# Kernel tuning notes

Measured on AMD Instinct MI355X. Metric: run time of the kernel, lower is better.

## Reference

```python
import jax, jax.numpy as jnp
import numpy as np

H = 8       # num_heads
D = 64      # inner_dim (per-head)
DM = 512    # input_dim == output_dim
EPS = 1e-5


def setup_inputs() -> dict:
    key = jax.random.key(0)
    ks = jax.random.split(key, 6)
    b, n = 2, 2048
    x = jax.random.normal(ks[0], (b, n, DM), dtype=jnp.float32)
    w_qkv = jax.random.normal(ks[1], (DM, 3 * H * D), dtype=jnp.float32) * (DM ** -0.5)
    head_mix = jax.random.normal(ks[2], (H, H), dtype=jnp.float32)
    ln_h_g = jnp.ones((H,), jnp.float32)
    ln_h_b = jnp.zeros((H,), jnp.float32)
    w_out = jax.random.normal(ks[3], (H * D, DM), dtype=jnp.float32) * ((H * D) ** -0.5)
    b_out = jnp.zeros((DM,), jnp.float32)
    ln_o_g = jnp.ones((DM,), jnp.float32)
    ln_o_b = jnp.zeros((DM,), jnp.float32)
    return {"x": x, "w_qkv": w_qkv, "head_mix": head_mix,
            "ln_h_g": ln_h_g, "ln_h_b": ln_h_b,
            "w_out": w_out, "b_out": b_out,
            "ln_o_g": ln_o_g, "ln_o_b": ln_o_b}


def reference(x, w_qkv, head_mix, ln_h_g, ln_h_b, w_out, b_out, ln_o_g, ln_o_b):
    b, n, _ = x.shape
    scale = D ** -0.5
    qkv = x @ w_qkv                                   # [b, n, 3*H*D]
    q, k, v = jnp.split(qkv, 3, axis=-1)
    def heads(t):
        return t.reshape(b, n, H, D).transpose(0, 2, 1, 3)  # [b, H, n, D]
    q, k, v = heads(q), heads(k), heads(v)
    dots = jnp.einsum('bhid,bhjd->bhij', q, k) * scale
    attn = jax.nn.softmax(dots, axis=-1)
    # talking-heads mix: bhij,hg->bgij
    attn = jnp.einsum('bhij,hg->bgij', attn, head_mix)
    # LayerNorm over the head axis (axis=1)
    mu = attn.mean(axis=1, keepdims=True)
    var = attn.var(axis=1, keepdims=True)
    attn = (attn - mu) * jax.lax.rsqrt(var + EPS)
    attn = attn * ln_h_g[None, :, None, None] + ln_h_b[None, :, None, None]
    out = jnp.einsum('bhij,bhjd->bhid', attn, v)      # [b, H, n, D]
    out = out.transpose(0, 2, 1, 3).reshape(b, n, H * D)
    out = out @ w_out + b_out                         # [b, n, DM]
    # LayerNorm over feature dim
    mo = out.mean(axis=-1, keepdims=True)
    vo = out.var(axis=-1, keepdims=True)
    out = (out - mo) * jax.lax.rsqrt(vo + EPS) * ln_o_g + ln_o_b
    out = (x + out).sum(axis=1)                       # [b, DM]
    return out, attn
```

## Files before the change

### kernel.cpp

```cpp
#include <hip/hip_runtime.h>
#include <hip/hip_bf16.h>

typedef __attribute__((ext_vector_type(8)))  short short8;
typedef __attribute__((ext_vector_type(16))) float f32x16;

#define LOG2E 1.44269504088896f
#define CS (0.125f * LOG2E)

static __device__ __forceinline__ short f2b(float f) {
  union { __hip_bfloat16 h; short s; } u; u.h = __float2bfloat16(f); return u.s;
}
static __device__ __forceinline__ f32x16 zf16() {
  f32x16 z;
#pragma unroll
  for (int i = 0; i < 16; ++i) z[i] = 0.f;
  return z;
}
static __device__ __forceinline__ f32x16 mfma32(short8 a, short8 b, f32x16 c) {
  return __builtin_amdgcn_mfma_f32_32x32x16_bf16(a, b, c, 0, 0, 0);
}

__global__ void k_convert(const float* __restrict__ x, const float* __restrict__ wqkv,
                          const float* __restrict__ wout,
                          short* __restrict__ xb, short* __restrict__ wqkvT,
                          short* __restrict__ woutT) {
  const int NX = 2 * 2048 * 512;
  const int NW = 512 * 1536;
  const int NO = 512 * 512;
  int i = blockIdx.x * 256 + threadIdx.x;
  if (i < NX) {
    xb[i] = f2b(x[i]);
  } else if (i < NX + NW) {
    int o = i - NX; int n = o >> 9; int k = o & 511;
    wqkvT[o] = f2b(wqkv[k * 1536 + n]);
  } else if (i < NX + NW + NO) {
    int o = i - NX - NW; int n = o >> 9; int k = o & 511;
    woutT[o] = f2b(wout[k * 512 + n]);
  }
}

__global__ void k_xsum(const float* __restrict__ x, float* __restrict__ outacc) {
  int blk = blockIdx.x;
  int b = blk >> 4, ch = blk & 15;
  int t = threadIdx.x;
  int f = t * 2;
  float s0 = 0.f, s1 = 0.f;
  const float* base = x + ((size_t)b * 2048 + (size_t)ch * 128) * 512;
  for (int r = 0; r < 128; ++r) {
    float2 v = *(const float2*)(base + (size_t)r * 512 + f);
    s0 += v.x; s1 += v.y;
  }
  atomicAdd(&outacc[b * 512 + f], s0);
  atomicAdd(&outacc[b * 512 + f + 1], s1);
}

__launch_bounds__(256)
__global__ void k_qkv(const short* __restrict__ xb, const short* __restrict__ wqkvT,
                      short* __restrict__ qg, short* __restrict__ kg,
                      short* __restrict__ vtmp) {
  __shared__ __align__(16) short As[128 * 64];
  __shared__ __align__(16) short Bs[128 * 64];
  int bx = blockIdx.x & 31;
  int by = blockIdx.x >> 5;
  int row0 = bx << 7, col0 = by << 7;
  int t = threadIdx.x, w = t >> 6, l = t & 63, li = l & 31, hi = l >> 5;
  int wr = w >> 1, wc = w & 1;
  f32x16 acc[2][2];
#pragma unroll
  for (int mi = 0; mi < 2; ++mi)
#pragma unroll
    for (int ni = 0; ni < 2; ++ni) acc[mi][ni] = zf16();

  for (int k0 = 0; k0 < 512; k0 += 64) {
    __syncthreads();
#pragma unroll
    for (int it = 0; it < 4; ++it) {
      int idx = t + it * 256;
      int r = idx >> 3, pc = idx & 7;
      int4 va = *(const int4*)(xb + (size_t)(row0 + r) * 512 + k0 + pc * 8);
      int dsto = (r * 128 + pc * 16) ^ ((r & 7) << 4);
      *(int4*)((char*)As + dsto) = va;
      int4 vb = *(const int4*)(wqkvT + (size_t)(col0 + r) * 512 + k0 + pc * 8);
      *(int4*)((char*)Bs + dsto) = vb;
    }
    __syncthreads();
#pragma unroll
    for (int kk = 0; kk < 4; ++kk) {
      short8 af[2], bfv[2];
#pragma unroll
      for (int mi = 0; mi < 2; ++mi) {
        int row = wr * 64 + mi * 32 + li;
        int byteo = (row * 128 + (kk * 2 + hi) * 16) ^ ((row & 7) << 4);
        af[mi] = *(const short8*)((char*)As + byteo);
      }
#pragma unroll
      for (int ni = 0; ni < 2; ++ni) {
        int col = wc * 64 + ni * 32 + li;
        int byteo = (col * 128 + (kk * 2 + hi) * 16) ^ ((col & 7) << 4);
        bfv[ni] = *(const short8*)((char*)Bs + byteo);
      }
#pragma unroll
      for (int mi = 0; mi < 2; ++mi)
#pragma unroll
        for (int ni = 0; ni < 2; ++ni)
          acc[mi][ni] = mfma32(af[mi], bfv[ni], acc[mi][ni]);
    }
  }
#pragma unroll
  for (int mi = 0; mi < 2; ++mi)
#pragma unroll
    for (int ni = 0; ni < 2; ++ni) {
      int colb = col0 + wc * 64 + ni * 32 + li;
      int sect = colb >> 9, rem = colb & 511, h = rem >> 6, d = rem & 63;
      short* dst = sect == 0 ? qg : (sect == 1 ? kg : vtmp);
#pragma unroll
      for (int r = 0; r < 16; ++r) {
        int row = row0 + wr * 64 + mi * 32 + ((r & 3) + ((r >> 2) << 3) + (hi << 2));
        int b = row >> 11, nn = row & 2047;
        dst[(((size_t)(b * 8 + h) * 2048 + nn) << 6) + d] = f2b(acc[mi][ni][r]);
      }
    }
}

__global__ void k_vt(const short* __restrict__ vtmp, short* __restrict__ vt) {
  __shared__ __align__(16) short tile[64 * 72];
  int blk = blockIdx.x;
  int bh = blk >> 5;
  int n0 = (blk & 31) << 6;
  int t = threadIdx.x;
#pragma unroll
  for (int it = 0; it < 2; ++it) {
    int idx = (t + it * 256) * 8;
    int r = idx >> 6, c = idx & 63;
    int4 v = *(const int4*)(vtmp + ((size_t)bh * 2048 + n0 + r) * 64 + c);
    *(int4*)(&tile[r * 72 + c]) = v;
  }
  __syncthreads();
#pragma unroll
  for (int it = 0; it < 2; ++it) {
    int idx = (t + it * 256) * 8;
    int d = idx >> 6, nn = idx & 63;
    short8 o;
#pragma unroll
    for (int j = 0; j < 8; ++j) o[j] = tile[(nn + j) * 72 + d];
    *(short8*)(vt + ((size_t)bh * 64 + d) * 2048 + n0 + nn) = o;
  }
}

__launch_bounds__(256)
__global__ void k_stats(const short* __restrict__ qg, const short* __restrict__ kg,
                        float* __restrict__ ml) {
  int w = threadIdx.x >> 6, l = threadIdx.x & 63, li = l & 31, hi = l >> 5;
  int wt = blockIdx.x * 4 + w;
  int b = wt >> 9, rem = wt & 511, h = rem >> 6, it = rem & 63;
  size_t bh = (size_t)(b * 8 + h) * 2048;
  int i = it * 32 + li;
  short8 q4[4];
#pragma unroll
  for (int kk = 0; kk < 4; ++kk)
    q4[kk] = *(const short8*)(qg + (bh + i) * 64 + kk * 16 + hi * 8);
  float m2 = -1e30f, ls = 0.f;
  for (int jt = 0; jt < 64; ++jt) {
    f32x16 s = zf16();
#pragma unroll
    for (int kk = 0; kk < 4; ++kk) {
      short8 kf = *(const short8*)(kg + (bh + jt * 32 + li) * 64 + kk * 16 + hi * 8);
      s = mfma32(kf, q4[kk], s);
    }
    float sv[16];
    float tm = -1e30f;
#pragma unroll
    for (int r = 0; r < 16; ++r) { sv[r] = s[r] * CS; tm = fmaxf(tm, sv[r]); }
    float mn = fmaxf(m2, tm);
    float acc = 0.f;
#pragma unroll
    for (int r = 0; r < 16; ++r) acc += exp2f(sv[r] - mn);
    ls = ls * exp2f(m2 - mn) + acc;
    m2 = mn;
  }
  float om = __shfl_xor(m2, 32, 64);
  float ol = __shfl_xor(ls, 32, 64);
  float mf = fmaxf(m2, om);
  float lf = ls * exp2f(m2 - mf) + ol * exp2f(om - mf);
  if (hi == 0) {
    float2 v = make_float2(mf, lf);
    *(float2*)(ml + (bh + i) * 2) = v;
  }
}

__launch_bounds__(512)
__global__ void k_attn(const short* __restrict__ qg, const short* __restrict__ kg,
                       const short* __restrict__ vt, const float* __restrict__ ml,
                       const float* __restrict__ mixg, const float* __restrict__ lnhg,
                       const float* __restrict__ lnhb, float* __restrict__ attn,
                       float* __restrict__ oh) {
  __shared__ __align__(16) float p_lds[8 * 32 * 33];
  __shared__ __align__(16) short a_lds[8 * 32 * 40];
  int t = threadIdx.x;
  int w = t >> 6, l = t & 63, li = l & 31, hi = l >> 5;
  int blk = blockIdx.x;
  int jg = blk & 3, itile = (blk >> 2) & 63, b = blk >> 8;
  int i0 = itile * 32;
  int h = w;
  size_t bh = (size_t)(b * 8 + h) * 2048;

  float mixr[64];
#pragma unroll
  for (int z = 0; z < 64; ++z) mixr[z] = mixg[z];
  float lg[8], lbv[8];
#pragma unroll
  for (int g = 0; g < 8; ++g) { lg[g] = lnhg[g]; lbv[g] = lnhb[g]; }

  short8 q4[4];
#pragma unroll
  for (int kk = 0; kk < 4; ++kk)
    q4[kk] = *(const short8*)(qg + (bh + i0 + li) * 64 + kk * 16 + hi * 8);
  float2 mlv = *(const float2*)(ml + (bh + i0 + li) * 2);
  float mI = mlv.x;
  float rl = 1.0f / mlv.y;

  f32x16 oacc[2];
  oacc[0] = zf16(); oacc[1] = zf16();

  int jj = t & 31;
  int ipb = (t >> 5) & 15;

  for (int jt = 0; jt < 16; ++jt) {
    int j0 = jg * 512 + jt * 32;
    f32x16 s = zf16();
#pragma unroll
    for (int kk = 0; kk < 4; ++kk) {
      short8 kf = *(const short8*)(kg + (bh + j0 + li) * 64 + kk * 16 + hi * 8);
      s = mfma32(kf, q4[kk], s);
    }
#pragma unroll
    for (int r = 0; r < 16; ++r) {
      float p = exp2f(fmaf(s[r], CS, -mI)) * rl;
      int jr = (r & 3) + ((r >> 2) << 3) + (hi << 2);
      p_lds[(h * 32 + jr) * 33 + li] = p;
    }
    __syncthreads();
#pragma unroll
    for (int pp = 0; pp < 2; ++pp) {
      int ip = ipb + pp * 16;
      float ph[8];
#pragma unroll
      for (int g = 0; g < 8; ++g) ph[g] = p_lds[(g * 32 + jj) * 33 + ip];
      float a[8];
#pragma unroll
      for (int g = 0; g < 8; ++g) {
        float a2 = 0.f;
#pragma unroll
        for (int hh = 0; hh < 8; ++hh) a2 = fmaf(ph[hh], mixr[hh * 8 + g], a2);
        a[g] = a2;
      }
      float mu = 0.f;
#pragma unroll
      for (int g = 0; g < 8; ++g) mu += a[g];
      mu *= 0.125f;
      float var = 0.f;
#pragma unroll
      for (int g = 0; g < 8; ++g) { float d2 = a[g] - mu; var = fmaf(d2, d2, var); }
      var *= 0.125f;
      float rs = rsqrtf(var + 1e-5f);
#pragma unroll
      for (int g = 0; g < 8; ++g) {
        float y = (a[g] - mu) * rs * lg[g] + lbv[g];
        attn[((size_t)(b * 8 + g) * 2048 + (size_t)(i0 + ip)) * 2048 + j0 + jj] = y;
        a_lds[(g * 32 + ip) * 40 + jj] = f2b(y);
      }
    }
    __syncthreads();
#pragma unroll
    for (int ks = 0; ks < 2; ++ks) {
      short8 af = *(const short8*)(&a_lds[(h * 32 + li) * 40 + ks * 16 + hi * 8]);
#pragma unroll
      for (int dt = 0; dt < 2; ++dt) {
        short8 vf = *(const short8*)(vt + ((size_t)(b * 8 + h) * 64 + dt * 32 + li) * 2048 + j0 + ks * 16 + hi * 8);
        oacc[dt] = mfma32(af, vf, oacc[dt]);
      }
    }
  }
#pragma unroll
  for (int dt = 0; dt < 2; ++dt)
#pragma unroll
    for (int r = 0; r < 16; ++r) {
      int ri = (r & 3) + ((r >> 2) << 3) + (hi << 2);
      atomicAdd(&oh[((size_t)(b * 2048 + i0 + ri)) * 512 + h * 64 + dt * 32 + li], oacc[dt][r]);
    }
}

__launch_bounds__(512)
__global__ void k_epi(const float* __restrict__ oh, const short* __restrict__ woutT,
                      const float* __restrict__ bo, const float* __restrict__ logv,
                      const float* __restrict__ lob, float* __restrict__ dout) {
  __shared__ __align__(16) short As[64 * 64];
  __shared__ float lnsum[64][4];
  __shared__ float lnsq[64][4];
  __shared__ float zsum[512];
  int t = threadIdx.x, w = t >> 6, l = t & 63, li = l & 31, hi = l >> 5;
  int rb = w >> 2, cb = w & 3;
  int m0 = blockIdx.x * 64;
  zsum[t] = 0.f;
  f32x16 acc[4];
#pragma unroll
  for (int ni = 0; ni < 4; ++ni) acc[ni] = zf16();

  for (int k0 = 0; k0 < 512; k0 += 64) {
    __syncthreads();
    {
      int r = t >> 3, c = (t & 7) * 8;
      float4 v0 = *(const float4*)(oh + (size_t)(m0 + r) * 512 + k0 + c);
      float4 v1 = *(const float4*)(oh + (size_t)(m0 + r) * 512 + k0 + c + 4);
      short8 o;
      o[0] = f2b(v0.x); o[1] = f2b(v0.y); o[2] = f2b(v0.z); o[3] = f2b(v0.w);
      o[4] = f2b(v1.x); o[5] = f2b(v1.y); o[6] = f2b(v1.z); o[7] = f2b(v1.w);
      int byteo = (r * 128 + c * 2) ^ ((r & 7) << 4);
      *(short8*)((char*)As + byteo) = o;
    }
    __syncthreads();
#pragma unroll
    for (int kk = 0; kk < 4; ++kk) {
      int rowA = rb * 32 + li;
      int byteo = (rowA * 128 + (kk * 2 + hi) * 16) ^ ((rowA & 7) << 4);
      short8 af = *(const short8*)((char*)As + byteo);
#pragma unroll
      for (int ni = 0; ni < 4; ++ni) {
        int n = cb * 128 + ni * 32 + li;
        short8 bfr = *(const short8*)(woutT + (size_t)n * 512 + k0 + kk * 16 + hi * 8);
        acc[ni] = mfma32(af, bfr, acc[ni]);
      }
    }
  }
  float bias[4], gg[4], b2[4];
#pragma unroll
  for (int ni = 0; ni < 4; ++ni) {
    int n = cb * 128 + ni * 32 + li;
    bias[ni] = bo[n]; gg[ni] = logv[n]; b2[ni] = lob[n];
  }
#pragma unroll
  for (int ni = 0; ni < 4; ++ni)
#pragma unroll
    for (int r = 0; r < 16; ++r) acc[ni][r] += bias[ni];

#pragma unroll
  for (int r = 0; r < 16; ++r) {
    float s = 0.f, q2 = 0.f;
#pragma unroll
    for (int ni = 0; ni < 4; ++ni) { float v = acc[ni][r]; s += v; q2 = fmaf(v, v, q2); }
    for (int d2 = 1; d2 < 32; d2 <<= 1) { s += __shfl_xor(s, d2); q2 += __shfl_xor(q2, d2); }
    int rw = rb * 32 + (r & 3) + ((r >> 2) << 3) + (hi << 2);
    if (li == 0) { lnsum[rw][cb] = s; lnsq[rw][cb] = q2; }
  }
  __syncthreads();
  float zp[4] = {0.f, 0.f, 0.f, 0.f};
#pragma unroll
  for (int r = 0; r < 16; ++r) {
    int rw = rb * 32 + (r & 3) + ((r >> 2) << 3) + (hi << 2);
    float s = lnsum[rw][0] + lnsum[rw][1] + lnsum[rw][2] + lnsum[rw][3];
    float q2 = lnsq[rw][0] + lnsq[rw][1] + lnsq[rw][2] + lnsq[rw][3];
    float mu = s * (1.f / 512.f);
    float var = q2 * (1.f / 512.f) - mu * mu;
    float rs = rsqrtf(var + 1e-5f);
#pragma unroll
    for (int ni = 0; ni < 4; ++ni) {
      float y = (acc[ni][r] - mu) * rs * gg[ni] + b2[ni];
      zp[ni] += y;
    }
  }
#pragma unroll
  for (int ni = 0; ni < 4; ++ni) zp[ni] += __shfl_xor(zp[ni], 32);
  if (hi == 0) {
#pragma unroll
    for (int ni = 0; ni < 4; ++ni) atomicAdd(&zsum[cb * 128 + ni * 32 + li], zp[ni]);
  }
  __syncthreads();
  int bsel = m0 >> 11;
  atomicAdd(&dout[bsel * 512 + t], zsum[t]);
}

extern "C" void kernel_launch(void* const* d_in, const int* in_sizes, int n_in,
                              void* d_out, int out_size, void* d_ws, size_t ws_size,
                              hipStream_t stream) {
  const float* x    = (const float*)d_in[0];
  const float* wqkv = (const float*)d_in[1];
  const float* mixg = (const float*)d_in[2];
  const float* lnhg = (const float*)d_in[3];
  const float* lnhb = (const float*)d_in[4];
  const float* wout = (const float*)d_in[5];
  const float* bo   = (const float*)d_in[6];
  const float* logv = (const float*)d_in[7];
  const float* lob  = (const float*)d_in[8];
  float* dout = (float*)d_out;
  char* ws = (char*)d_ws;
  short* xb    = (short*)(ws + 0);
  short* wqkvT = (short*)(ws + 4194304);
  short* woutT = (short*)(ws + 5767168);
  short* qg    = (short*)(ws + 6291456);
  short* kg    = (short*)(ws + 10485760);
  short* vtmp  = (short*)(ws + 14680064);
  short* vt    = (short*)(ws + 18874368);
  float* ml    = (float*)(ws + 23068672);
  float* oh    = (float*)(ws + 23330816);

  hipMemsetAsync(dout, 0, 1024 * sizeof(float), stream);
  hipMemsetAsync(oh, 0, (size_t)2 * 2048 * 512 * 4, stream);

  k_convert<<<12288, 256, 0, stream>>>(x, wqkv, wout, xb, wqkvT, woutT);
  k_xsum<<<32, 256, 0, stream>>>(x, dout);
  k_qkv<<<384, 256, 0, stream>>>(xb, wqkvT, qg, kg, vtmp);
  k_vt<<<512, 256, 0, stream>>>(vtmp, vt);
  k_stats<<<256, 256, 0, stream>>>(qg, kg, ml);
  k_attn<<<512, 512, 0, stream>>>(qg, kg, vt, ml, mixg, lnhg, lnhb, dout + 1024, oh);
  k_epi<<<64, 512, 0, stream>>>(oh, woutT, bo, logv, lob, dout);
}
```

Before: 555.1 us.

## Parallelize stats over waves, replace oh atomics with partial buffers, vectorize attn stores

```diff
diff --git a/kernel.cpp b/kernel.cpp
--- a/kernel.cpp
+++ b/kernel.cpp
@@ -18,6 +18,9 @@
 }
 static __device__ __forceinline__ f32x16 mfma32(short8 a, short8 b, f32x16 c) {
   return __builtin_amdgcn_mfma_f32_32x32x16_bf16(a, b, c, 0, 0, 0);
+}
+static __device__ __forceinline__ float rfl(float v) {
+  return __int_as_float(__builtin_amdgcn_readfirstlane(__float_as_int(v)));
 }
 
 __global__ void k_convert(const float* __restrict__ x, const float* __restrict__ wqkv,
@@ -150,9 +153,10 @@
 __launch_bounds__(256)
 __global__ void k_stats(const short* __restrict__ qg, const short* __restrict__ kg,
                         float* __restrict__ ml) {
-  int w = threadIdx.x >> 6, l = threadIdx.x & 63, li = l & 31, hi = l >> 5;
-  int wt = blockIdx.x * 4 + w;
-  int b = wt >> 9, rem = wt & 511, h = rem >> 6, it = rem & 63;
+  __shared__ float red[4][32][2];
+  int t = threadIdx.x, w = t >> 6, l = t & 63, li = l & 31, hi = l >> 5;
+  int blk = blockIdx.x;
+  int b = blk >> 9, rem = blk & 511, h = rem >> 6, it = rem & 63;
   size_t bh = (size_t)(b * 8 + h) * 2048;
   int i = it * 32 + li;
   short8 q4[4];
@@ -160,7 +164,7 @@
   for (int kk = 0; kk < 4; ++kk)
     q4[kk] = *(const short8*)(qg + (bh + i) * 64 + kk * 16 + hi * 8);
   float m2 = -1e30f, ls = 0.f;
-  for (int jt = 0; jt < 64; ++jt) {
+  for (int jt = w * 16; jt < w * 16 + 16; ++jt) {
     f32x16 s = zf16();
 #pragma unroll
     for (int kk = 0; kk < 4; ++kk) {
@@ -182,13 +186,22 @@
   float ol = __shfl_xor(ls, 32, 64);
   float mf = fmaxf(m2, om);
   float lf = ls * exp2f(m2 - mf) + ol * exp2f(om - mf);
-  if (hi == 0) {
-    float2 v = make_float2(mf, lf);
-    *(float2*)(ml + (bh + i) * 2) = v;
-  }
-}
-
-__launch_bounds__(512)
+  if (hi == 0) { red[w][li][0] = mf; red[w][li][1] = lf; }
+  __syncthreads();
+  if (t < 32) {
+    float m = red[0][t][0], s = red[0][t][1];
+#pragma unroll
+    for (int ww = 1; ww < 4; ++ww) {
+      float m1 = red[ww][t][0], s1 = red[ww][t][1];
+      float mn = fmaxf(m, m1);
+      s = s * exp2f(m - mn) + s1 * exp2f(m1 - mn);
+      m = mn;
+    }
+    *(float2*)(ml + (bh + it * 32 + t) * 2) = make_float2(m, s);
+  }
+}
+
+__launch_bounds__(512, 4)
 __global__ void k_attn(const short* __restrict__ qg, const short* __restrict__ kg,
                        const short* __restrict__ vt, const float* __restrict__ ml,
                        const float* __restrict__ mixg, const float* __restrict__ lnhg,
@@ -206,24 +219,23 @@
 
   float mixr[64];
 #pragma unroll
-  for (int z = 0; z < 64; ++z) mixr[z] = mixg[z];
+  for (int z = 0; z < 64; ++z) mixr[z] = rfl(mixg[z]);
   float lg[8], lbv[8];
 #pragma unroll
-  for (int g = 0; g < 8; ++g) { lg[g] = lnhg[g]; lbv[g] = lnhb[g]; }
+  for (int g = 0; g < 8; ++g) { lg[g] = rfl(lnhg[g]); lbv[g] = rfl(lnhb[g]); }
 
   short8 q4[4];
 #pragma unroll
   for (int kk = 0; kk < 4; ++kk)
     q4[kk] = *(const short8*)(qg + (bh + i0 + li) * 64 + kk * 16 + hi * 8);
   float2 mlv = *(const float2*)(ml + (bh + i0 + li) * 2);
-  float mI = mlv.x;
-  float rl = 1.0f / mlv.y;
+  float c0 = -(mlv.x + __log2f(mlv.y));
 
   f32x16 oacc[2];
   oacc[0] = zf16(); oacc[1] = zf16();
 
-  int jj = t & 31;
-  int ipb = (t >> 5) & 15;
+  int ii = t >> 4;
+  int jp = (t & 15) * 2;
 
   for (int jt = 0; jt < 16; ++jt) {
     int j0 = jg * 512 + jt * 32;
@@ -235,39 +247,49 @@
     }
 #pragma unroll
     for (int r = 0; r < 16; ++r) {
-      float p = exp2f(fmaf(s[r], CS, -mI)) * rl;
+      float p = exp2f(fmaf(s[r], CS, c0));
       int jr = (r & 3) + ((r >> 2) << 3) + (hi << 2);
       p_lds[(h * 32 + jr) * 33 + li] = p;
     }
     __syncthreads();
-#pragma unroll
-    for (int pp = 0; pp < 2; ++pp) {
-      int ip = ipb + pp * 16;
-      float ph[8];
-#pragma unroll
-      for (int g = 0; g < 8; ++g) ph[g] = p_lds[(g * 32 + jj) * 33 + ip];
-      float a[8];
+    {
+      float pf[8][2], a[8][2];
 #pragma unroll
       for (int g = 0; g < 8; ++g) {
-        float a2 = 0.f;
-#pragma unroll
-        for (int hh = 0; hh < 8; ++hh) a2 = fmaf(ph[hh], mixr[hh * 8 + g], a2);
-        a[g] = a2;
-      }
-      float mu = 0.f;
-#pragma unroll
-      for (int g = 0; g < 8; ++g) mu += a[g];
-      mu *= 0.125f;
-      float var = 0.f;
-#pragma unroll
-      for (int g = 0; g < 8; ++g) { float d2 = a[g] - mu; var = fmaf(d2, d2, var); }
-      var *= 0.125f;
-      float rs = rsqrtf(var + 1e-5f);
+        pf[g][0] = p_lds[(g * 32 + jp) * 33 + ii];
+        pf[g][1] = p_lds[(g * 32 + jp + 1) * 33 + ii];
+      }
 #pragma unroll
       for (int g = 0; g < 8; ++g) {
-        float y = (a[g] - mu) * rs * lg[g] + lbv[g];
-        attn[((size_t)(b * 8 + g) * 2048 + (size_t)(i0 + ip)) * 2048 + j0 + jj] = y;
-        a_lds[(g * 32 + ip) * 40 + jj] = f2b(y);
+#pragma unroll
+        for (int jb = 0; jb < 2; ++jb) {
+          float a2 = 0.f;
+#pragma unroll
+          for (int hh = 0; hh < 8; ++hh) a2 = fmaf(pf[hh][jb], mixr[hh * 8 + g], a2);
+          a[g][jb] = a2;
+        }
+      }
+      float mu[2], rs[2];
+#pragma unroll
+      for (int jb = 0; jb < 2; ++jb) {
+        float m2 = 0.f;
+#pragma unroll
+        for (int g = 0; g < 8; ++g) m2 += a[g][jb];
+        m2 *= 0.125f;
+        float var = 0.f;
+#pragma unroll
+        for (int g = 0; g < 8; ++g) { float d2 = a[g][jb] - m2; var = fmaf(d2, d2, var); }
+        var *= 0.125f;
+        mu[jb] = m2; rs[jb] = rsqrtf(var + 1e-5f);
+      }
+#pragma unroll
+      for (int g = 0; g < 8; ++g) {
+        float y0 = (a[g][0] - mu[0]) * rs[0] * lg[g] + lbv[g];
+        float y1 = (a[g][1] - mu[1]) * rs[1] * lg[g] + lbv[g];
+        *(float2*)(&attn[((size_t)(b * 8 + g) * 2048 + (size_t)(i0 + ii)) * 2048 + j0 + jp]) =
+            make_float2(y0, y1);
+        unsigned int pk = (unsigned short)f2b(y0) | ((unsigned int)(unsigned short)f2b(y1) << 16);
+        *(unsigned int*)(&a_lds[(g * 32 + ii) * 40 + jp]) = pk;
       }
     }
     __syncthreads();
@@ -281,12 +303,13 @@
       }
     }
   }
+  float* ohp = oh + (size_t)jg * (2 * 2048 * 512);
 #pragma unroll
   for (int dt = 0; dt < 2; ++dt)
 #pragma unroll
     for (int r = 0; r < 16; ++r) {
       int ri = (r & 3) + ((r >> 2) << 3) + (hi << 2);
-      atomicAdd(&oh[((size_t)(b * 2048 + i0 + ri)) * 512 + h * 64 + dt * 32 + li], oacc[dt][r]);
+      ohp[((size_t)(b * 2048 + i0 + ri)) * 512 + h * 64 + dt * 32 + li] = oacc[dt][r];
     }
 }
 
@@ -294,85 +317,88 @@
 __global__ void k_epi(const float* __restrict__ oh, const short* __restrict__ woutT,
                       const float* __restrict__ bo, const float* __restrict__ logv,
                       const float* __restrict__ lob, float* __restrict__ dout) {
-  __shared__ __align__(16) short As[64 * 64];
-  __shared__ float lnsum[64][4];
-  __shared__ float lnsq[64][4];
+  __shared__ __align__(16) short As[32 * 64];
+  __shared__ float lnsum[32][8];
+  __shared__ float lnsq[32][8];
   __shared__ float zsum[512];
+  const size_t NPART = (size_t)2 * 2048 * 512;
   int t = threadIdx.x, w = t >> 6, l = t & 63, li = l & 31, hi = l >> 5;
-  int rb = w >> 2, cb = w & 3;
-  int m0 = blockIdx.x * 64;
-  zsum[t] = 0.f;
-  f32x16 acc[4];
-#pragma unroll
-  for (int ni = 0; ni < 4; ++ni) acc[ni] = zf16();
+  int m0 = blockIdx.x * 32;
+  f32x16 acc[2];
+  acc[0] = zf16(); acc[1] = zf16();
 
   for (int k0 = 0; k0 < 512; k0 += 64) {
     __syncthreads();
     {
-      int r = t >> 3, c = (t & 7) * 8;
-      float4 v0 = *(const float4*)(oh + (size_t)(m0 + r) * 512 + k0 + c);
-      float4 v1 = *(const float4*)(oh + (size_t)(m0 + r) * 512 + k0 + c + 4);
-      short8 o;
-      o[0] = f2b(v0.x); o[1] = f2b(v0.y); o[2] = f2b(v0.z); o[3] = f2b(v0.w);
-      o[4] = f2b(v1.x); o[5] = f2b(v1.y); o[6] = f2b(v1.z); o[7] = f2b(v1.w);
+      int r = t >> 4, c = (t & 15) * 4;
+      size_t off = (size_t)(m0 + r) * 512 + k0 + c;
+      float4 v = *(const float4*)(oh + off);
+#pragma unroll
+      for (int p = 1; p < 4; ++p) {
+        float4 v2 = *(const float4*)(oh + p * NPART + off);
+        v.x += v2.x; v.y += v2.y; v.z += v2.z; v.w += v2.w;
+      }
+      short o[4] = { f2b(v.x), f2b(v.y), f2b(v.z), f2b(v.w) };
       int byteo = (r * 128 + c * 2) ^ ((r & 7) << 4);
-      *(short8*)((char*)As + byteo) = o;
+      *(int2*)((char*)As + byteo) = *(int2*)o;
     }
     __syncthreads();
 #pragma unroll
     for (int kk = 0; kk < 4; ++kk) {
-      int rowA = rb * 32 + li;
-      int byteo = (rowA * 128 + (kk * 2 + hi) * 16) ^ ((rowA & 7) << 4);
+      int byteo = (li * 128 + (kk * 2 + hi) * 16) ^ ((li & 7) << 4);
       short8 af = *(const short8*)((char*)As + byteo);
 #pragma unroll
-      for (int ni = 0; ni < 4; ++ni) {
-        int n = cb * 128 + ni * 32 + li;
+      for (int ni = 0; ni < 2; ++ni) {
+        int n = w * 64 + ni * 32 + li;
         short8 bfr = *(const short8*)(woutT + (size_t)n * 512 + k0 + kk * 16 + hi * 8);
         acc[ni] = mfma32(af, bfr, acc[ni]);
       }
     }
   }
-  float bias[4], gg[4], b2[4];
-#pragma unroll
-  for (int ni = 0; ni < 4; ++ni) {
-    int n = cb * 128 + ni * 32 + li;
+  float bias[2], gg[2], b2[2];
+#pragma unroll
+  for (int ni = 0; ni < 2; ++ni) {
+    int n = w * 64 + ni * 32 + li;
     bias[ni] = bo[n]; gg[ni] = logv[n]; b2[ni] = lob[n];
   }
 #pragma unroll
-  for (int ni = 0; ni < 4; ++ni)
+  for (int ni = 0; ni < 2; ++ni)
 #pragma unroll
     for (int r = 0; r < 16; ++r) acc[ni][r] += bias[ni];
 
 #pragma unroll
   for (int r = 0; r < 16; ++r) {
+    float s = acc[0][r] + acc[1][r];
+    float q2 = fmaf(acc[0][r], acc[0][r], acc[1][r] * acc[1][r]);
+    for (int d2 = 1; d2 < 32; d2 <<= 1) { s += __shfl_xor(s, d2); q2 += __shfl_xor(q2, d2); }
+    int row = (r & 3) + ((r >> 2) << 3) + (hi << 2);
+    if (li == 0) { lnsum[row][w] = s; lnsq[row][w] = q2; }
+  }
+  __syncthreads();
+  if (t < 32) {
     float s = 0.f, q2 = 0.f;
 #pragma unroll
-    for (int ni = 0; ni < 4; ++ni) { float v = acc[ni][r]; s += v; q2 = fmaf(v, v, q2); }
-    for (int d2 = 1; d2 < 32; d2 <<= 1) { s += __shfl_xor(s, d2); q2 += __shfl_xor(q2, d2); }
-    int rw = rb * 32 + (r & 3) + ((r >> 2) << 3) + (hi << 2);
-    if (li == 0) { lnsum[rw][cb] = s; lnsq[rw][cb] = q2; }
+    for (int ww = 0; ww < 8; ++ww) { s += lnsum[t][ww]; q2 += lnsq[t][ww]; }
+    float m2 = s * (1.f / 512.f);
+    float var = q2 * (1.f / 512.f) - m2 * m2;
+    lnsum[t][0] = m2;
+    lnsq[t][0] = rsqrtf(var + 1e-5f);
   }
   __syncthreads();
-  float zp[4] = {0.f, 0.f, 0.f, 0.f};
+  float zc[2] = {0.f, 0.f};
 #pragma unroll
   for (int r = 0; r < 16; ++r) {
-    int rw = rb * 32 + (r & 3) + ((r >> 2) << 3) + (hi << 2);
-    float s = lnsum[rw][0] + lnsum[rw][1] + lnsum[rw][2] + lnsum[rw][3];
-    float q2 = lnsq[rw][0] + lnsq[rw][1] + lnsq[rw][2] + lnsq[rw][3];
-    float mu = s * (1.f / 512.f);
-    float var = q2 * (1.f / 512.f) - mu * mu;
-    float rs = rsqrtf(var + 1e-5f);
-#pragma unroll
-    for (int ni = 0; ni < 4; ++ni) {
-      float y = (acc[ni][r] - mu) * rs * gg[ni] + b2[ni];
-      zp[ni] += y;
-    }
-  }
-#pragma unroll
-  for (int ni = 0; ni < 4; ++ni) zp[ni] += __shfl_xor(zp[ni], 32);
+    int row = (r & 3) + ((r >> 2) << 3) + (hi << 2);
+    float m2 = lnsum[row][0], rs = lnsq[row][0];
+#pragma unroll
+    for (int ni = 0; ni < 2; ++ni)
+      zc[ni] += (acc[ni][r] - m2) * rs * gg[ni] + b2[ni];
+  }
+#pragma unroll
+  for (int ni = 0; ni < 2; ++ni) zc[ni] += __shfl_xor(zc[ni], 32);
   if (hi == 0) {
 #pragma unroll
-    for (int ni = 0; ni < 4; ++ni) atomicAdd(&zsum[cb * 128 + ni * 32 + li], zp[ni]);
+    for (int ni = 0; ni < 2; ++ni) zsum[w * 64 + ni * 32 + li] = zc[ni];
   }
   __syncthreads();
   int bsel = m0 >> 11;
@@ -404,13 +430,12 @@
   float* oh    = (float*)(ws + 23330816);
 
   hipMemsetAsync(dout, 0, 1024 * sizeof(float), stream);
-  hipMemsetAsync(oh, 0, (size_t)2 * 2048 * 512 * 4, stream);
 
   k_convert<<<12288, 256, 0, stream>>>(x, wqkv, wout, xb, wqkvT, woutT);
   k_xsum<<<32, 256, 0, stream>>>(x, dout);
   k_qkv<<<384, 256, 0, stream>>>(xb, wqkvT, qg, kg, vtmp);
   k_vt<<<512, 256, 0, stream>>>(vtmp, vt);
-  k_stats<<<256, 256, 0, stream>>>(qg, kg, ml);
+  k_stats<<<1024, 256, 0, stream>>>(qg, kg, ml);
   k_attn<<<512, 512, 0, stream>>>(qg, kg, vt, ml, mixg, lnhg, lnhb, dout + 1024, oh);
-  k_epi<<<64, 512, 0, stream>>>(oh, woutT, bo, logv, lob, dout);
-}
+  k_epi<<<128, 512, 0, stream>>>(oh, woutT, bo, logv, lob, dout);
+}
```

Result: faster. 452.4 us (-18.5%).
